# Performance work log

Measured on AMD Instinct MI355X. Metric: run time of the kernel, lower is better.

The kernel has to match this reference:

```python
import jax, jax.numpy as jnp
import numpy as np

B, S, H = 32, 2048, 1024

def setup_inputs() -> dict:
    key = jax.random.key(0)
    k1, k2, k3, k4, k5 = jax.random.split(key, 5)
    hidden = jax.random.normal(k1, (1, B, H), dtype=jnp.float32)
    encoder_outputs = jax.random.normal(k2, (B, S, H), dtype=jnp.float32)
    # nn.Linear(2H, H): weight [H, 2H], bias [H]
    W_attn = jax.random.normal(k3, (H, 2 * H), dtype=jnp.float32) * (1.0 / np.sqrt(2 * H))
    b_attn = jax.random.normal(k4, (H,), dtype=jnp.float32) * 0.01
    # nn.Linear(H, 1, bias=False): weight [1, H] -> stored as [H]
    v = jax.random.normal(k5, (H,), dtype=jnp.float32) * (1.0 / np.sqrt(H))
    return {"hidden": hidden, "encoder_outputs": encoder_outputs,
            "W_attn": W_attn, "b_attn": b_attn, "v": v}

def reference(hidden, encoder_outputs, W_attn, b_attn, v):
    # hidden: [1, B, H] -> [B, H]; encoder_outputs: [B, S, H]
    h = hidden[0]  # [B, H]
    # cat((hidden_repeated, enc), -1) @ W_attn.T == h @ Wh.T + enc @ We.T
    Wh = W_attn[:, :H]   # [H, H] acts on hidden part
    We = W_attn[:, H:]   # [H, H] acts on encoder part
    h_proj = jnp.einsum('bh,oh->bo', h, Wh)                    # [B, H]
    e_proj = jnp.einsum('bsh,oh->bso', encoder_outputs, We)    # [B, S, H]
    energy = jnp.tanh(e_proj + h_proj[:, None, :] + b_attn)    # [B, S, H]
    attention = jnp.einsum('bsh,h->bs', energy, v)             # [B, S]
    return jax.nn.softmax(attention, axis=1)
```

## Files before the change

kernel.cpp:

```cpp
#include <hip/hip_runtime.h>
#include <hip/hip_bf16.h>
#include <cstdint>


#define HDIM 1024
#define SDIM 2048
#define MTOT 65536

typedef __attribute__((ext_vector_type(8))) short short8;
typedef __attribute__((ext_vector_type(4))) float floatx4;

__device__ __forceinline__ unsigned short f2bf(float f) {
    unsigned int u = __float_as_uint(f);
    u += 0x7fffu + ((u >> 16) & 1u);
    return (unsigned short)(u >> 16);
}
__device__ __forceinline__ unsigned int pack2(float a, float b) {
    return (unsigned int)f2bf(a) | ((unsigned int)f2bf(b) << 16);
}
__device__ __forceinline__ float fast_tanh(float x) {
    float e2 = __expf(2.f * x);
    return 1.f - 2.f * __builtin_amdgcn_rcpf(e2 + 1.f);
}

__global__ __launch_bounds__(256) void prep(const float* __restrict__ W,
                                            unsigned short* __restrict__ Wbf2,
                                            const float* __restrict__ hid,
                                            const float* __restrict__ bias,
                                            float* __restrict__ c) {
    __shared__ float red[4][32];
    if (blockIdx.x < 512) {
        int T = blockIdx.x * 256 + threadIdx.x;
        int n  = T >> 7;
        int k8 = T & 127;
        int k  = k8 * 8;
        const float4* src = (const float4*)(W + (size_t)n * 2048 + 1024 + k);
        float4 f0 = src[0], f1 = src[1];
        int jt = n >> 4, lc = n & 15, kc = k8 >> 2, g = k8 & 3;
        uint4 u;
        u.x = pack2(f0.x, f0.y); u.y = pack2(f0.z, f0.w);
        u.z = pack2(f1.x, f1.y); u.w = pack2(f1.z, f1.w);
        *(uint4*)(Wbf2 + (size_t)(jt * 32 + kc) * 512 + (g * 16 + lc) * 8) = u;
    } else {
        const int o = blockIdx.x - 512;
        const int wave = threadIdx.x >> 6, lane = threadIdx.x & 63;
        const int k = wave * 256 + lane * 4;
        const float4 wv = *(const float4*)(W + (size_t)o * 2048 + k);
        float acc[32];
#pragma unroll
        for (int b = 0; b < 32; ++b) {
            const float4 h = *(const float4*)(hid + b * HDIM + k);
            acc[b] = wv.x * h.x + wv.y * h.y + wv.z * h.z + wv.w * h.w;
        }
#pragma unroll
        for (int b = 0; b < 32; ++b) {
            float x = acc[b];
            for (int off = 32; off; off >>= 1) x += __shfl_xor(x, off);
            if (lane == 0) red[wave][b] = x;
        }
        __syncthreads();
        if (threadIdx.x < 32) {
            int b = threadIdx.x;
            c[b * HDIM + o] = red[0][b] + red[1][b] + red[2][b] + red[3][b] + bias[o];
        }
    }
}

#define PHN 8
#define PHK 128

__global__ __launch_bounds__(512, 2) void attn_fused(const float* __restrict__ enc,
                                                     const unsigned short* __restrict__ Wbf2,
                                                     const float* __restrict__ c,
                                                     const float* __restrict__ v,
                                                     float* __restrict__ part) {
    __shared__ __align__(16) unsigned short slab[2][128 * 128];

    const int tid  = threadIdx.x;
    const int lane = tid & 63;
    const int wave = tid >> 6;
    const int grp  = lane >> 4;
    const int lc   = lane & 15;

    const int strip = blockIdx.x >> 1;
    const int nhalf = blockIdx.x & 1;
    const int m0 = strip * 128;
    const int b  = m0 >> 11;
    const int cb = nhalf * 512 + wave * 64;

    const int s_kk   = (lane & 31) * 4;
    const int s_rsub = lane >> 5;
    const int s_c16  = (lane & 31) >> 1;
    const int s_b8   = lane & 1;

    floatx4 acc[8][4];
#pragma unroll
    for (int i = 0; i < 8; ++i)
#pragma unroll
        for (int j = 0; j < 4; ++j) acc[i][j] = (floatx4){0.f, 0.f, 0.f, 0.f};

    const short8* Bfr = (const short8*)Wbf2;
    const int jt0 = nhalf * 32 + wave * 4;

    float4 ld[8];
#pragma unroll
    for (int q = 0; q < 8; ++q) {
        int row = wave * 16 + q * 2 + s_rsub;
        ld[q] = *(const float4*)(enc + (size_t)(m0 + row) * HDIM + s_kk);
    }
#pragma unroll
    for (int q = 0; q < 8; ++q) {
        int row  = wave * 16 + q * 2 + s_rsub;
        int slot = s_c16 ^ (row & 7);
        uint2 u = {pack2(ld[q].x, ld[q].y), pack2(ld[q].z, ld[q].w)};
        *(uint2*)(&slab[0][row * 128 + slot * 8 + s_b8 * 4]) = u;
    }

    short8 bf[4], bn[4];
#pragma unroll
    for (int j = 0; j < 4; ++j)
        bf[j] = Bfr[(size_t)((jt0 + j) * 32 + 0) * 64 + lane];

#pragma unroll 1
    for (int p = 0; p < PHN; ++p) {
        __syncthreads();

        if (p < PHN - 1) {
#pragma unroll
            for (int q = 0; q < 8; ++q) {
                int row = wave * 16 + q * 2 + s_rsub;
                ld[q] = *(const float4*)(enc + (size_t)(m0 + row) * HDIM +
                                         (p + 1) * PHK + s_kk);
            }
        }

        const unsigned short* sl = slab[p & 1];
#pragma unroll
        for (int s = 0; s < 4; ++s) {
            const int kc = s;
            short8 af[8];
#pragma unroll
            for (int i = 0; i < 8; ++i) {
                int row  = i * 16 + lc;
                int slot = (kc * 4 + grp) ^ (lc & 7);
                af[i] = *(const short8*)(sl + row * 128 + slot * 8);
            }
            {
                const int kc2 = (s + 1) & 3;
                const int pn  = (s < 3) ? p : ((p < PHN - 1) ? p + 1 : p);
#pragma unroll
                for (int j = 0; j < 4; ++j)
                    bn[j] = Bfr[(size_t)((jt0 + j) * 32 + pn * 4 + kc2) * 64 + lane];
            }
#pragma unroll
            for (int i = 0; i < 8; ++i)
#pragma unroll
                for (int j = 0; j < 4; ++j)
                    acc[i][j] = __builtin_amdgcn_mfma_f32_16x16x32_bf16(
                        af[i], bf[j], acc[i][j], 0, 0, 0);
#pragma unroll
            for (int j = 0; j < 4; ++j) bf[j] = bn[j];
        }

        if (p < PHN - 1) {
#pragma unroll
            for (int q = 0; q < 8; ++q) {
                int row  = wave * 16 + q * 2 + s_rsub;
                int slot = s_c16 ^ (row & 7);
                uint2 u = {pack2(ld[q].x, ld[q].y), pack2(ld[q].z, ld[q].w)};
                *(uint2*)(&slab[(p + 1) & 1][row * 128 + slot * 8 + s_b8 * 4]) = u;
            }
        }
    }

    float rowsum[8][4];
#pragma unroll
    for (int i = 0; i < 8; ++i)
#pragma unroll
        for (int r = 0; r < 4; ++r) rowsum[i][r] = 0.f;

#pragma unroll
    for (int j = 0; j < 4; ++j) {
        const int n  = cb + j * 16 + lc;
        const float vn = v[n];
        const float cv = c[b * HDIM + n];
#pragma unroll
        for (int i = 0; i < 8; ++i)
#pragma unroll
            for (int r = 0; r < 4; ++r)
                rowsum[i][r] = fmaf(fast_tanh(acc[i][j][r] + cv), vn,
                                    rowsum[i][r]);
    }

    __syncthreads();
    float* red = (float*)slab;
#pragma unroll
    for (int i = 0; i < 8; ++i)
#pragma unroll
        for (int r = 0; r < 4; ++r) {
            float x = rowsum[i][r];
            x += __shfl_xor(x, 8);
            x += __shfl_xor(x, 4);
            x += __shfl_xor(x, 2);
            x += __shfl_xor(x, 1);
            if (lc == 0) red[wave * 128 + i * 16 + grp * 4 + r] = x;
        }
    __syncthreads();
    if (tid < 128) {
        float ssum = 0.f;
#pragma unroll
        for (int w = 0; w < 8; ++w) ssum += red[w * 128 + tid];
        part[(size_t)nhalf * MTOT + m0 + tid] = ssum;
    }
}

__global__ __launch_bounds__(256) void softmax_k(const float* __restrict__ part,
                                                 float* __restrict__ out) {
    __shared__ float wred[4];
    const int bb = blockIdx.x;
    const int tid = threadIdx.x;
    const int wave = tid >> 6, lane = tid & 63;

    float vals[8];
    float lmax = -INFINITY;
#pragma unroll
    for (int q = 0; q < 8; ++q) {
        const size_t idx = (size_t)bb * SDIM + q * 256 + tid;
        vals[q] = part[idx] + part[(size_t)MTOT + idx];
        lmax = fmaxf(lmax, vals[q]);
    }
    for (int off = 32; off; off >>= 1) lmax = fmaxf(lmax, __shfl_xor(lmax, off));
    if (lane == 0) wred[wave] = lmax;
    __syncthreads();
    lmax = fmaxf(fmaxf(wred[0], wred[1]), fmaxf(wred[2], wred[3]));
    __syncthreads();

    float e[8];
    float s = 0.f;
#pragma unroll
    for (int q = 0; q < 8; ++q) {
        e[q] = __expf(vals[q] - lmax);
        s += e[q];
    }
    for (int off = 32; off; off >>= 1) s += __shfl_xor(s, off);
    if (lane == 0) wred[wave] = s;
    __syncthreads();
    s = wred[0] + wred[1] + wred[2] + wred[3];
    const float inv = 1.f / s;
#pragma unroll
    for (int q = 0; q < 8; ++q)
        out[(size_t)bb * SDIM + q * 256 + tid] = e[q] * inv;
}

extern "C" void kernel_launch(void* const* d_in, const int* in_sizes, int n_in,
                              void* d_out, int out_size, void* d_ws, size_t ws_size,
                              hipStream_t stream) {
    const float* hidden = (const float*)d_in[0];
    const float* enc    = (const float*)d_in[1];
    const float* W      = (const float*)d_in[2];
    const float* battn  = (const float*)d_in[3];
    const float* v      = (const float*)d_in[4];
    float* out = (float*)d_out;

    char* ws = (char*)d_ws;
    float* c             = (float*)ws;
    float* part          = (float*)(ws + (128 << 10));
    unsigned short* Wbf2 = (unsigned short*)(ws + (640 << 10));

    hipLaunchKernelGGL(prep,       dim3(1536), dim3(256), 0, stream, W, Wbf2, hidden, battn, c);
    hipLaunchKernelGGL(attn_fused, dim3(1024), dim3(512), 0, stream, enc, Wbf2, c, v, part);
    hipLaunchKernelGGL(softmax_k,  dim3(32),   dim3(256), 0, stream, part, out);
}
```

Baseline: 491.9 us.

## Interleave encoder staging with MFMA steps, deepen B prefetch, and remap block order

Splits the encoder tile load into four small batches whose LDS writes and next global loads are spread across the four MFMA sub-steps, instead of one big load before and one big store after. This cuts live registers and overlaps the bf16 conversion and stores with compute. The weight fragments are now prefetched two k-steps ahead from a double buffer. Blocks are also remapped so the two N halves of a strip and neighbouring strips are scheduled differently for better L2 locality. The cost is more complex scheduling, with some risk of extra stalls from LDS writes landing mid-compute.

```diff
diff --git a/kernel.cpp b/kernel.cpp
--- a/kernel.cpp
+++ b/kernel.cpp
@@ -82,61 +82,76 @@
     const int grp  = lane >> 4;
     const int lc   = lane & 15;
 
-    const int strip = blockIdx.x >> 1;
-    const int nhalf = blockIdx.x & 1;
+    const int j     = blockIdx.x;
+    const int strip = (j & 7) * 64 + (j >> 4);
+    const int nhalf = (j >> 3) & 1;
     const int m0 = strip * 128;
     const int b  = m0 >> 11;
     const int cb = nhalf * 512 + wave * 64;
 
-    const int s_kk   = (lane & 31) * 4;
-    const int s_rsub = lane >> 5;
-    const int s_c16  = (lane & 31) >> 1;
-    const int s_b8   = lane & 1;
+    const int s_row4 = lane >> 4;
+    const int s_c16  = lane & 15;
+    const float* encw = enc + (size_t)(m0 + wave * 16 + s_row4) * HDIM + s_c16 * 8;
 
     floatx4 acc[8][4];
 #pragma unroll
     for (int i = 0; i < 8; ++i)
 #pragma unroll
-        for (int j = 0; j < 4; ++j) acc[i][j] = (floatx4){0.f, 0.f, 0.f, 0.f};
+        for (int jj = 0; jj < 4; ++jj) acc[i][jj] = (floatx4){0.f, 0.f, 0.f, 0.f};
 
     const short8* Bfr = (const short8*)Wbf2;
     const int jt0 = nhalf * 32 + wave * 4;
 
-    float4 ld[8];
-#pragma unroll
-    for (int q = 0; q < 8; ++q) {
-        int row = wave * 16 + q * 2 + s_rsub;
-        ld[q] = *(const float4*)(enc + (size_t)(m0 + row) * HDIM + s_kk);
-    }
-#pragma unroll
-    for (int q = 0; q < 8; ++q) {
-        int row  = wave * 16 + q * 2 + s_rsub;
-        int slot = s_c16 ^ (row & 7);
-        uint2 u = {pack2(ld[q].x, ld[q].y), pack2(ld[q].z, ld[q].w)};
-        *(uint2*)(&slab[0][row * 128 + slot * 8 + s_b8 * 4]) = u;
-    }
-
-    short8 bf[4], bn[4];
-#pragma unroll
-    for (int j = 0; j < 4; ++j)
-        bf[j] = Bfr[(size_t)((jt0 + j) * 32 + 0) * 64 + lane];
+    float4 ldq[2][2];
+    const int w_rowb = wave * 16 + s_row4;
+
+#define ISSUE_BATCH(par, q, pn)                                               \
+    {                                                                         \
+        const float* src = encw + (size_t)(q) * 4 * HDIM + (pn) * PHK;        \
+        ldq[par][0] = *(const float4*)(src);                                  \
+        ldq[par][1] = *(const float4*)(src + 4);                              \
+    }
+#define WRITE_BATCH(par, q, buf)                                              \
+    {                                                                         \
+        int row  = w_rowb + (q) * 4;                                          \
+        int slot = s_c16 ^ (row & 7);                                         \
+        uint4 u;                                                              \
+        u.x = pack2(ldq[par][0].x, ldq[par][0].y);                            \
+        u.y = pack2(ldq[par][0].z, ldq[par][0].w);                            \
+        u.z = pack2(ldq[par][1].x, ldq[par][1].y);                            \
+        u.w = pack2(ldq[par][1].z, ldq[par][1].w);                            \
+        *(uint4*)(&slab[buf][row * 128 + slot * 8]) = u;                      \
+    }
+
+    ISSUE_BATCH(0, 0, 0)
+    ISSUE_BATCH(1, 1, 0)
+    WRITE_BATCH(0, 0, 0)
+    ISSUE_BATCH(0, 2, 0)
+    WRITE_BATCH(1, 1, 0)
+    ISSUE_BATCH(1, 3, 0)
+    WRITE_BATCH(0, 2, 0)
+    WRITE_BATCH(1, 3, 0)
+
+    short8 Bv[2][4];
+#pragma unroll
+    for (int jj = 0; jj < 4; ++jj) {
+        Bv[0][jj] = Bfr[(size_t)((jt0 + jj) * 32 + 0) * 64 + lane];
+        Bv[1][jj] = Bfr[(size_t)((jt0 + jj) * 32 + 1) * 64 + lane];
+    }
 
 #pragma unroll 1
     for (int p = 0; p < PHN; ++p) {
         __syncthreads();
 
         if (p < PHN - 1) {
-#pragma unroll
-            for (int q = 0; q < 8; ++q) {
-                int row = wave * 16 + q * 2 + s_rsub;
-                ld[q] = *(const float4*)(enc + (size_t)(m0 + row) * HDIM +
-                                         (p + 1) * PHK + s_kk);
-            }
+            ISSUE_BATCH(0, 0, p + 1)
+            ISSUE_BATCH(1, 1, p + 1)
         }
 
         const unsigned short* sl = slab[p & 1];
 #pragma unroll
         for (int s = 0; s < 4; ++s) {
+            const int t  = p * 4 + s;
             const int kc = s;
             short8 af[8];
 #pragma unroll
@@ -145,30 +160,23 @@
                 int slot = (kc * 4 + grp) ^ (lc & 7);
                 af[i] = *(const short8*)(sl + row * 128 + slot * 8);
             }
+#pragma unroll
+            for (int i = 0; i < 8; ++i)
+#pragma unroll
+                for (int jj = 0; jj < 4; ++jj)
+                    acc[i][jj] = __builtin_amdgcn_mfma_f32_16x16x32_bf16(
+                        af[i], Bv[s & 1][jj], acc[i][jj], 0, 0, 0);
             {
-                const int kc2 = (s + 1) & 3;
-                const int pn  = (s < 3) ? p : ((p < PHN - 1) ? p + 1 : p);
-#pragma unroll
-                for (int j = 0; j < 4; ++j)
-                    bn[j] = Bfr[(size_t)((jt0 + j) * 32 + pn * 4 + kc2) * 64 + lane];
+                const int kcg = (t + 2 < 32) ? (t + 2) : 31;
+#pragma unroll
+                for (int jj = 0; jj < 4; ++jj)
+                    Bv[s & 1][jj] = Bfr[(size_t)((jt0 + jj) * 32 + kcg) * 64 + lane];
             }
-#pragma unroll
-            for (int i = 0; i < 8; ++i)
-#pragma unroll
-                for (int j = 0; j < 4; ++j)
-                    acc[i][j] = __builtin_amdgcn_mfma_f32_16x16x32_bf16(
-                        af[i], bf[j], acc[i][j], 0, 0, 0);
-#pragma unroll
-            for (int j = 0; j < 4; ++j) bf[j] = bn[j];
-        }
-
-        if (p < PHN - 1) {
-#pragma unroll
-            for (int q = 0; q < 8; ++q) {
-                int row  = wave * 16 + q * 2 + s_rsub;
-                int slot = s_c16 ^ (row & 7);
-                uint2 u = {pack2(ld[q].x, ld[q].y), pack2(ld[q].z, ld[q].w)};
-                *(uint2*)(&slab[(p + 1) & 1][row * 128 + slot * 8 + s_b8 * 4]) = u;
+            if (p < PHN - 1) {
+                if (s == 0)      { WRITE_BATCH(0, 0, (p + 1) & 1) ISSUE_BATCH(0, 2, p + 1) }
+                else if (s == 1) { WRITE_BATCH(1, 1, (p + 1) & 1) ISSUE_BATCH(1, 3, p + 1) }
+                else if (s == 2) { WRITE_BATCH(0, 2, (p + 1) & 1) }
+                else             { WRITE_BATCH(1, 3, (p + 1) & 1) }
             }
         }
     }
@@ -180,15 +188,15 @@
         for (int r = 0; r < 4; ++r) rowsum[i][r] = 0.f;
 
 #pragma unroll
-    for (int j = 0; j < 4; ++j) {
-        const int n  = cb + j * 16 + lc;
+    for (int jj = 0; jj < 4; ++jj) {
+        const int n  = cb + jj * 16 + lc;
         const float vn = v[n];
         const float cv = c[b * HDIM + n];
 #pragma unroll
         for (int i = 0; i < 8; ++i)
 #pragma unroll
             for (int r = 0; r < 4; ++r)
-                rowsum[i][r] = fmaf(fast_tanh(acc[i][j][r] + cv), vn,
+                rowsum[i][r] = fmaf(fast_tanh(acc[i][jj][r] + cv), vn,
                                     rowsum[i][r]);
     }
 
@@ -212,6 +220,8 @@
         for (int w = 0; w < 8; ++w) ssum += red[w * 128 + tid];
         part[(size_t)nhalf * MTOT + m0 + tid] = ssum;
     }
+#undef ISSUE_BATCH
+#undef WRITE_BATCH
 }
 
 __global__ __launch_bounds__(256) void softmax_k(const float* __restrict__ part,
```

After: 559.0 us. +13.6%, slower.
